# Kernel optimization log

Measured on AMD Instinct MI355X. Metric: run time of the kernel, lower is better.

## Reference

```python
import jax, jax.numpy as jnp
import numpy as np

NUM_LEVELS = 16
LEVEL_DIM = 2
BASE_RES = 16
PER_LEVEL_SCALE = 2.0
LOG2_HASHMAP = 19
INPUT_DIM = 3
N_POINTS = 2_000_000
B = 262144


def _compute_offsets():
    offsets = []
    off = 0
    max_params = 2 ** LOG2_HASHMAP
    for i in range(NUM_LEVELS):
        res = int(np.ceil(BASE_RES * PER_LEVEL_SCALE ** i))
        p = min(max_params, (res + 1) ** INPUT_DIM)  # align_corners=False -> res+1 verts per axis
        p = int(np.ceil(p / 8) * 8)
        offsets.append(off)
        off += p
    offsets.append(off)
    return offsets

OFFSETS = _compute_offsets()
TOTAL_PARAMS = OFFSETS[-1]  # 7131240
PRIMES = (1, 2654435761, 805459861)  # instant-ngp fast_hash primes for D=3
CORNER_BITS = np.array([[(c >> d) & 1 for d in range(3)] for c in range(8)], dtype=np.int32)  # [8,3]


def _build_table(embeddings, fs_embeddings, scatter_index):
    # scatter_add point embeddings (and counts) into grid vertices, then blend
    sums = jnp.zeros((TOTAL_PARAMS, LEVEL_DIM), embeddings.dtype).at[scatter_index].add(embeddings)
    counts = jnp.zeros((TOTAL_PARAMS,), embeddings.dtype).at[scatter_index].add(1.0)
    sel = jnp.minimum(counts, 1.0)[:, None]
    num = jnp.maximum(counts, 1.0)[:, None]
    return (sums / num) * sel + fs_embeddings * (1.0 - sel)


def _grid_encode(x, table):
    # x: [B,3] in [0,1]; table: [TOTAL_PARAMS, C]. Multi-res hash grid, linear interp,
    # align_corners=False (matches torch-ngp grid_encode CUDA kernel).
    S = np.log2(PER_LEVEL_SCALE)
    bits_i = jnp.asarray(CORNER_BITS)                 # [8,3] int
    bits_f = jnp.asarray(CORNER_BITS, dtype=x.dtype)  # [8,3] float
    outs = []
    for level in range(NUM_LEVELS):
        scale = np.exp2(level * S) * BASE_RES - 1.0
        resolution = int(np.ceil(scale)) + 1
        hashmap_size = OFFSETS[level + 1] - OFFSETS[level]
        pos = x * scale + 0.5  # align_corners=False offset
        pos_grid = jnp.floor(pos)
        frac = pos - pos_grid                                  # [B,3]
        corner = pos_grid.astype(jnp.int32)[:, None, :] + bits_i  # [B,8,3]
        stride = (resolution + 1) ** 3
        if stride > hashmap_size:
            # hashed level: xor of per-dim prime products, uint32 wraparound
            cu = corner.astype(jnp.uint32)
            idx = (cu[..., 0] * jnp.uint32(PRIMES[0])) ^ \
                  (cu[..., 1] * jnp.uint32(PRIMES[1])) ^ \
                  (cu[..., 2] * jnp.uint32(PRIMES[2]))
            idx = (idx % jnp.uint32(hashmap_size)).astype(jnp.int32)
        else:
            # dense level: row-major index with stride (res+1)
            r1 = resolution + 1
            idx = (corner[..., 0] + corner[..., 1] * r1 + corner[..., 2] * (r1 * r1)) % hashmap_size
        vals = table[idx + OFFSETS[level]]  # [B,8,C] gather
        w = jnp.prod(jnp.where(bits_f > 0, frac[:, None, :], 1.0 - frac[:, None, :]), axis=-1)  # [B,8]
        outs.append(jnp.einsum('bk,bkc->bc', w, vals))
    return jnp.concatenate(outs, axis=-1)  # [B, L*C]


def setup_inputs() -> dict:
    key = jax.random.key(0)
    k1, k2, k3, k4 = jax.random.split(key, 4)
    std = 1e-4  # reset_parameters() uniform(-1e-4, 1e-4)
    inputs = jax.random.uniform(k1, (B, 3), jnp.float32, minval=-1.0, maxval=1.0)
    embeddings = jax.random.uniform(k2, (N_POINTS, LEVEL_DIM), jnp.float32, minval=-std, maxval=std)
    fs_embeddings = jax.random.uniform(k3, (TOTAL_PARAMS, LEVEL_DIM), jnp.float32, minval=-std, maxval=std)
    scatter_index = jax.random.randint(k4, (N_POINTS,), 0, TOTAL_PARAMS, dtype=jnp.int32)
    return {"inputs": inputs, "embeddings": embeddings, "fs_embeddings": fs_embeddings,
            "scatter_index": scatter_index, "bound": 1}


def reference(inputs, embeddings, fs_embeddings, scatter_index, bound):
    table = _build_table(embeddings, fs_embeddings, scatter_index)
    x = (inputs + bound) / (2.0 * bound)  # map to [0,1]
    return _grid_encode(x, table)  # [B, NUM_LEVELS*LEVEL_DIM]
```

## Files before the change

kernel.cpp:

```cpp
#include <hip/hip_runtime.h>

#define TOTAL_PARAMS 7131240
#define NLEVELS 16
#define NB 262144
#define HASH_MASK 0x7FFFF

#define SF2 5115000.0f
#define CF 1e-4f

__constant__ int c_off[NLEVELS] = {
    0, 4920, 40864, 315496, 839784, 1364072, 1888360, 2412648,
    2936936, 3461224, 3985512, 4509800, 5034088, 5558376, 6082664, 6606952};

typedef float vfloat2 __attribute__((ext_vector_type(2)));
typedef float vfloat4 __attribute__((ext_vector_type(4)));
typedef unsigned vuint2 __attribute__((ext_vector_type(2)));
typedef int vint2 __attribute__((ext_vector_type(2)));

__global__ __launch_bounds__(256) void scatter_kernel(
    const vfloat4* __restrict__ emb2, const vint2* __restrict__ sidx2,
    unsigned* __restrict__ accum, int n) {
    int i = blockIdx.x * 256 + threadIdx.x;
    int base = i * 2;
    if (base >= n) return;
    if (base + 1 < n) {
        vint2 idx = __builtin_nontemporal_load(&sidx2[i]);
        vfloat4 e = __builtin_nontemporal_load(&emb2[i]);
        unsigned qx0 = __float2uint_rn((e.x + CF) * SF2);
        unsigned qy0 = __float2uint_rn((e.y + CF) * SF2);
        unsigned qx1 = __float2uint_rn((e.z + CF) * SF2);
        unsigned qy1 = __float2uint_rn((e.w + CF) * SF2);
        atomicAdd(&accum[idx.x], (1u << 28) | (qx0 << 14) | qy0);
        atomicAdd(&accum[idx.y], (1u << 28) | (qx1 << 14) | qy1);
    } else {
        const int* sidx = (const int*)sidx2;
        const vfloat2* emb = (const vfloat2*)emb2;
        int idx = sidx[base];
        vfloat2 e = emb[base];
        unsigned qx = __float2uint_rn((e.x + CF) * SF2);
        unsigned qy = __float2uint_rn((e.y + CF) * SF2);
        atomicAdd(&accum[idx], (1u << 28) | (qx << 14) | qy);
    }
}

__device__ __forceinline__ unsigned short f2bf(float f) {
    unsigned u = __builtin_bit_cast(unsigned, f);
    return (unsigned short)((u + 0x7FFFu + ((u >> 16) & 1u)) >> 16);
}

__global__ __launch_bounds__(256) void finalize_kernel(
    const unsigned* __restrict__ accum, const vfloat4* __restrict__ fs2,
    unsigned long long* __restrict__ table2, int npairs) {
    int i = blockIdx.x * 256 + threadIdx.x;
    if (i >= npairs) return;
    vuint2 a = __builtin_nontemporal_load((const vuint2*)(accum + 2 * i));
    unsigned c0 = a.x >> 28, c1 = a.y >> 28;
    vfloat4 f = {0.0f, 0.0f, 0.0f, 0.0f};
    if ((c0 == 0u) | (c1 == 0u)) f = __builtin_nontemporal_load(&fs2[i]);
    float rx0, ry0, rx1, ry1;
    if (c0 == 0u) {
        rx0 = f.x; ry0 = f.y;
    } else {
        float inv = 1.0f / ((float)c0 * SF2);
        rx0 = (float)((a.x >> 14) & 0x3FFFu) * inv - CF;
        ry0 = (float)(a.x & 0x3FFFu) * inv - CF;
    }
    if (c1 == 0u) {
        rx1 = f.z; ry1 = f.w;
    } else {
        float inv = 1.0f / ((float)c1 * SF2);
        rx1 = (float)((a.y >> 14) & 0x3FFFu) * inv - CF;
        ry1 = (float)(a.y & 0x3FFFu) * inv - CF;
    }
    unsigned lo = (unsigned)f2bf(rx0) | ((unsigned)f2bf(ry0) << 16);
    unsigned hi = (unsigned)f2bf(rx1) | ((unsigned)f2bf(ry1) << 16);
    table2[i] = (unsigned long long)lo | ((unsigned long long)hi << 32);
}

template <bool DENSE>
__device__ __forceinline__ vfloat2 level_interp(
    float px, float py, float pz, int l, const unsigned* __restrict__ table_bf) {
    int res = 16 << l;
    float scale = (float)(res - 1);
    float posx = px * scale + 0.5f;
    float posy = py * scale + 0.5f;
    float posz = pz * scale + 0.5f;
    float gx = floorf(posx), gy = floorf(posy), gz = floorf(posz);
    float fx = posx - gx, fy = posy - gy, fz = posz - gz;
    int ix = (int)gx, iy = (int)gy, iz = (int)gz;

    const unsigned* __restrict__ tb = table_bf + c_off[l];

    unsigned tyz[4];
    if (DENSE) {
        unsigned r1u = (unsigned)(res + 1);
        unsigned r1sq = r1u * r1u;
        unsigned ty0 = (unsigned)iy * r1u;
        unsigned tz0 = (unsigned)iz * r1sq;
        tyz[0] = ty0 + tz0;
        tyz[1] = ty0 + r1u + tz0;
        tyz[2] = ty0 + tz0 + r1sq;
        tyz[3] = ty0 + r1u + tz0 + r1sq;
    } else {
        unsigned ty0 = (unsigned)iy * 2654435761u;
        unsigned ty1 = ty0 + 2654435761u;
        unsigned tz0 = (unsigned)iz * 805459861u;
        unsigned tz1 = tz0 + 805459861u;
        tyz[0] = ty0 ^ tz0;
        tyz[1] = ty1 ^ tz0;
        tyz[2] = ty0 ^ tz1;
        tyz[3] = ty1 ^ tz1;
    }

    unsigned i0[4], i1[4];
    vuint2 P[4];
#pragma unroll
    for (int c = 0; c < 4; ++c) {
        if (DENSE) {
            i0[c] = tyz[c] + (unsigned)ix;
            i1[c] = i0[c] + 1u;
        } else {
            i0[c] = ((unsigned)ix ^ tyz[c]) & HASH_MASK;
            i1[c] = (((unsigned)ix + 1u) ^ tyz[c]) & HASH_MASK;
        }
        P[c] = *(const vuint2*)(tb + (i0[c] & ~1u));
    }
    unsigned vX[4];
#pragma unroll
    for (int c = 0; c < 4; ++c) {
        vX[c] = 0u;
        if (i1[c] != (i0[c] ^ 1u)) vX[c] = tb[i1[c]];
    }

    float wy0 = 1.0f - fy, wz0 = 1.0f - fz;
    float wyzv[4];
    wyzv[0] = wy0 * wz0;
    wyzv[1] = fy * wz0;
    wyzv[2] = wy0 * fz;
    wyzv[3] = fy * fz;
    float wx0 = 1.0f - fx;
    float ax = 0.0f, ay = 0.0f;
#pragma unroll
    for (int c = 0; c < 4; ++c) {
        unsigned lo = P[c].x, hi = P[c].y;
        bool odd = (i0[c] & 1u) != 0u;
        unsigned v0 = odd ? hi : lo;
        unsigned vo = odd ? lo : hi;
        unsigned v1 = (i1[c] == (i0[c] ^ 1u)) ? vo : vX[c];
        float v0x = __builtin_bit_cast(float, v0 << 16);
        float v0y = __builtin_bit_cast(float, v0 & 0xFFFF0000u);
        float v1x = __builtin_bit_cast(float, v1 << 16);
        float v1y = __builtin_bit_cast(float, v1 & 0xFFFF0000u);
        float w = wyzv[c];
        ax += w * (wx0 * v0x + fx * v1x);
        ay += w * (wx0 * v0y + fx * v1y);
    }
    vfloat2 r;
    r.x = ax;
    r.y = ay;
    return r;
}

__global__ __launch_bounds__(256) void encode_hash_kernel(
    const float* __restrict__ x, const int* __restrict__ bound_p,
    const unsigned* __restrict__ table_bf, vfloat2* __restrict__ lm) {
    int l = 15 - (blockIdx.x >> 10);
    int b = ((blockIdx.x & 1023) << 8) + threadIdx.x;

    float bound = (float)bound_p[0];
    float denom = 2.0f * bound;
    float px = (x[b * 3 + 0] + bound) / denom;
    float py = (x[b * 3 + 1] + bound) / denom;
    float pz = (x[b * 3 + 2] + bound) / denom;

    vfloat2 o = level_interp<false>(px, py, pz, l, table_bf);
    __builtin_nontemporal_store(o, &lm[(l - 3) * NB + b]);
}

__global__ __launch_bounds__(256) void finish_kernel(
    const float* __restrict__ x, const int* __restrict__ bound_p,
    const unsigned* __restrict__ table_bf, const vfloat2* __restrict__ lm,
    float* __restrict__ out) {
    int b = blockIdx.x * 256 + threadIdx.x;

    float bound = (float)bound_p[0];
    float denom = 2.0f * bound;
    float px = (x[b * 3 + 0] + bound) / denom;
    float py = (x[b * 3 + 1] + bound) / denom;
    float pz = (x[b * 3 + 2] + bound) / denom;

    float row[2 * NLEVELS];

#pragma unroll
    for (int lev = 0; lev < 13; ++lev) {
        vfloat2 v = lm[lev * NB + b];
        row[2 * (lev + 3)] = v.x;
        row[2 * (lev + 3) + 1] = v.y;
    }
#pragma unroll
    for (int l = 0; l < 3; ++l) {
        vfloat2 o = level_interp<true>(px, py, pz, l, table_bf);
        row[2 * l] = o.x;
        row[2 * l + 1] = o.y;
    }

    vfloat4* op = (vfloat4*)&out[b * 32];
#pragma unroll
    for (int k = 0; k < 8; ++k) {
        vfloat4 o;
        o.x = row[4 * k + 0];
        o.y = row[4 * k + 1];
        o.z = row[4 * k + 2];
        o.w = row[4 * k + 3];
        op[k] = o;
    }
}

extern "C" void kernel_launch(void* const* d_in, const int* in_sizes, int n_in,
                              void* d_out, int out_size, void* d_ws, size_t ws_size,
                              hipStream_t stream) {
    const float* x     = (const float*)d_in[0];
    const float* emb   = (const float*)d_in[1];
    const float* fs    = (const float*)d_in[2];
    const int*   sidx  = (const int*)d_in[3];
    const int*   bound = (const int*)d_in[4];

    unsigned* accum    = (unsigned*)d_ws;
    unsigned* table_bf = accum + TOTAL_PARAMS;
    vfloat2*  lm       = (vfloat2*)d_ws;

    int npts = in_sizes[3];
    int B = in_sizes[0] / 3;

    (void)hipMemsetAsync(d_ws, 0, (size_t)TOTAL_PARAMS * sizeof(unsigned), stream);

    int npair_pts = (npts + 1) / 2;
    scatter_kernel<<<(npair_pts + 255) / 256, 256, 0, stream>>>(
        (const vfloat4*)emb, (const vint2*)sidx, accum, npts);

    int npairs = TOTAL_PARAMS / 2;
    finalize_kernel<<<(npairs + 255) / 256, 256, 0, stream>>>(
        accum, (const vfloat4*)fs, (unsigned long long*)table_bf, npairs);

    encode_hash_kernel<<<13 * (B / 256), 256, 0, stream>>>(
        x, bound, table_bf, lm);

    finish_kernel<<<B / 256, 256, 0, stream>>>(
        x, bound, table_bf, lm, (float*)d_out);
}
```

Baseline: 330.1 us.

## Precompute normalized inputs, process two points per thread, simplify corner gathers

Folds input normalization into the scatter launch as extra blocks that write padded float4 normalized coordinates, so the encode and finish kernels load one aligned vector instead of three strided floats plus a divide. The hash encode kernel now handles two points per thread with explicit occupancy bounds, to raise memory-level parallelism on the random table gathers. The paired 64-bit gather with a conditional extra load is replaced by eight independent 32-bit loads, which removes branches but issues more load instructions. The trade is an extra workspace buffer and higher register pressure per thread.

```diff
diff --git a/kernel.cpp b/kernel.cpp
--- a/kernel.cpp
+++ b/kernel.cpp
@@ -17,9 +17,24 @@
 typedef unsigned vuint2 __attribute__((ext_vector_type(2)));
 typedef int vint2 __attribute__((ext_vector_type(2)));
 
-__global__ __launch_bounds__(256) void scatter_kernel(
+__global__ __launch_bounds__(256) void scatter_prep_kernel(
     const vfloat4* __restrict__ emb2, const vint2* __restrict__ sidx2,
-    unsigned* __restrict__ accum, int n) {
+    unsigned* __restrict__ accum, int n, int nsb,
+    const float* __restrict__ x, const int* __restrict__ bound_p,
+    vfloat4* __restrict__ xn, int B) {
+    if ((int)blockIdx.x >= nsb) {
+        int p = ((int)blockIdx.x - nsb) * 256 + threadIdx.x;
+        if (p >= B) return;
+        float bound = (float)bound_p[0];
+        float denom = 2.0f * bound;
+        vfloat4 o;
+        o.x = (x[p * 3 + 0] + bound) / denom;
+        o.y = (x[p * 3 + 1] + bound) / denom;
+        o.z = (x[p * 3 + 2] + bound) / denom;
+        o.w = 0.0f;
+        xn[p] = o;
+        return;
+    }
     int i = blockIdx.x * 256 + threadIdx.x;
     int base = i * 2;
     if (base >= n) return;
@@ -87,7 +102,7 @@
     float posz = pz * scale + 0.5f;
     float gx = floorf(posx), gy = floorf(posy), gz = floorf(posz);
     float fx = posx - gx, fy = posy - gy, fz = posz - gz;
-    int ix = (int)gx, iy = (int)gy, iz = (int)gz;
+    unsigned ix = (unsigned)(int)gx, iy = (unsigned)(int)gy, iz = (unsigned)(int)gz;
 
     const unsigned* __restrict__ tb = table_bf + c_off[l];
 
@@ -95,63 +110,41 @@
     if (DENSE) {
         unsigned r1u = (unsigned)(res + 1);
         unsigned r1sq = r1u * r1u;
-        unsigned ty0 = (unsigned)iy * r1u;
-        unsigned tz0 = (unsigned)iz * r1sq;
+        unsigned ty0 = iy * r1u, tz0 = iz * r1sq;
         tyz[0] = ty0 + tz0;
         tyz[1] = ty0 + r1u + tz0;
         tyz[2] = ty0 + tz0 + r1sq;
         tyz[3] = ty0 + r1u + tz0 + r1sq;
     } else {
-        unsigned ty0 = (unsigned)iy * 2654435761u;
-        unsigned ty1 = ty0 + 2654435761u;
-        unsigned tz0 = (unsigned)iz * 805459861u;
-        unsigned tz1 = tz0 + 805459861u;
+        unsigned ty0 = iy * 2654435761u, ty1 = ty0 + 2654435761u;
+        unsigned tz0 = iz * 805459861u, tz1 = tz0 + 805459861u;
         tyz[0] = ty0 ^ tz0;
         tyz[1] = ty1 ^ tz0;
         tyz[2] = ty0 ^ tz1;
         tyz[3] = ty1 ^ tz1;
     }
 
-    unsigned i0[4], i1[4];
-    vuint2 P[4];
-#pragma unroll
-    for (int c = 0; c < 4; ++c) {
-        if (DENSE) {
-            i0[c] = tyz[c] + (unsigned)ix;
-            i1[c] = i0[c] + 1u;
-        } else {
-            i0[c] = ((unsigned)ix ^ tyz[c]) & HASH_MASK;
-            i1[c] = (((unsigned)ix + 1u) ^ tyz[c]) & HASH_MASK;
-        }
-        P[c] = *(const vuint2*)(tb + (i0[c] & ~1u));
-    }
-    unsigned vX[4];
-#pragma unroll
-    for (int c = 0; c < 4; ++c) {
-        vX[c] = 0u;
-        if (i1[c] != (i0[c] ^ 1u)) vX[c] = tb[i1[c]];
+    unsigned v[8];
+#pragma unroll
+    for (int c = 0; c < 8; ++c) {
+        unsigned cx = ix + (unsigned)(c & 1);
+        unsigned idx;
+        if (DENSE) idx = cx + tyz[c >> 1];
+        else       idx = (cx ^ tyz[c >> 1]) & HASH_MASK;
+        v[c] = tb[idx];
     }
 
     float wy0 = 1.0f - fy, wz0 = 1.0f - fz;
-    float wyzv[4];
-    wyzv[0] = wy0 * wz0;
-    wyzv[1] = fy * wz0;
-    wyzv[2] = wy0 * fz;
-    wyzv[3] = fy * fz;
+    float wyz[4] = {wy0 * wz0, fy * wz0, wy0 * fz, fy * fz};
     float wx0 = 1.0f - fx;
     float ax = 0.0f, ay = 0.0f;
 #pragma unroll
-    for (int c = 0; c < 4; ++c) {
-        unsigned lo = P[c].x, hi = P[c].y;
-        bool odd = (i0[c] & 1u) != 0u;
-        unsigned v0 = odd ? hi : lo;
-        unsigned vo = odd ? lo : hi;
-        unsigned v1 = (i1[c] == (i0[c] ^ 1u)) ? vo : vX[c];
-        float v0x = __builtin_bit_cast(float, v0 << 16);
-        float v0y = __builtin_bit_cast(float, v0 & 0xFFFF0000u);
-        float v1x = __builtin_bit_cast(float, v1 << 16);
-        float v1y = __builtin_bit_cast(float, v1 & 0xFFFF0000u);
-        float w = wyzv[c];
+    for (int c2 = 0; c2 < 4; ++c2) {
+        float v0x = __builtin_bit_cast(float, v[2 * c2] << 16);
+        float v0y = __builtin_bit_cast(float, v[2 * c2] & 0xFFFF0000u);
+        float v1x = __builtin_bit_cast(float, v[2 * c2 + 1] << 16);
+        float v1y = __builtin_bit_cast(float, v[2 * c2 + 1] & 0xFFFF0000u);
+        float w = wyz[c2];
         ax += w * (wx0 * v0x + fx * v1x);
         ay += w * (wx0 * v0y + fx * v1y);
     }
@@ -161,33 +154,86 @@
     return r;
 }
 
-__global__ __launch_bounds__(256) void encode_hash_kernel(
-    const float* __restrict__ x, const int* __restrict__ bound_p,
-    const unsigned* __restrict__ table_bf, vfloat2* __restrict__ lm) {
-    int l = 15 - (blockIdx.x >> 10);
-    int b = ((blockIdx.x & 1023) << 8) + threadIdx.x;
-
-    float bound = (float)bound_p[0];
-    float denom = 2.0f * bound;
-    float px = (x[b * 3 + 0] + bound) / denom;
-    float py = (x[b * 3 + 1] + bound) / denom;
-    float pz = (x[b * 3 + 2] + bound) / denom;
-
-    vfloat2 o = level_interp<false>(px, py, pz, l, table_bf);
-    __builtin_nontemporal_store(o, &lm[(l - 3) * NB + b]);
-}
-
-__global__ __launch_bounds__(256) void finish_kernel(
-    const float* __restrict__ x, const int* __restrict__ bound_p,
-    const unsigned* __restrict__ table_bf, const vfloat2* __restrict__ lm,
-    float* __restrict__ out) {
+struct v2x2 { vfloat2 a, b; };
+
+__device__ __forceinline__ void hash_idx8(
+    float px, float py, float pz, float scale,
+    unsigned idx[8], float* fx, float* fy, float* fz) {
+    float posx = px * scale + 0.5f;
+    float posy = py * scale + 0.5f;
+    float posz = pz * scale + 0.5f;
+    float gx = floorf(posx), gy = floorf(posy), gz = floorf(posz);
+    *fx = posx - gx; *fy = posy - gy; *fz = posz - gz;
+    unsigned ix = (unsigned)(int)gx, iy = (unsigned)(int)gy, iz = (unsigned)(int)gz;
+    unsigned ty0 = iy * 2654435761u, ty1 = ty0 + 2654435761u;
+    unsigned tz0 = iz * 805459861u, tz1 = tz0 + 805459861u;
+    unsigned tyz[4] = {ty0 ^ tz0, ty1 ^ tz0, ty0 ^ tz1, ty1 ^ tz1};
+#pragma unroll
+    for (int c = 0; c < 8; ++c)
+        idx[c] = ((ix + (unsigned)(c & 1)) ^ tyz[c >> 1]) & HASH_MASK;
+}
+
+__device__ __forceinline__ vfloat2 wsum8(
+    const unsigned v[8], float fx, float fy, float fz) {
+    float wy0 = 1.0f - fy, wz0 = 1.0f - fz;
+    float wyz[4] = {wy0 * wz0, fy * wz0, wy0 * fz, fy * fz};
+    float wx0 = 1.0f - fx;
+    float ax = 0.0f, ay = 0.0f;
+#pragma unroll
+    for (int c2 = 0; c2 < 4; ++c2) {
+        float v0x = __builtin_bit_cast(float, v[2 * c2] << 16);
+        float v0y = __builtin_bit_cast(float, v[2 * c2] & 0xFFFF0000u);
+        float v1x = __builtin_bit_cast(float, v[2 * c2 + 1] << 16);
+        float v1y = __builtin_bit_cast(float, v[2 * c2 + 1] & 0xFFFF0000u);
+        float w = wyz[c2];
+        ax += w * (wx0 * v0x + fx * v1x);
+        ay += w * (wx0 * v0y + fx * v1y);
+    }
+    vfloat2 r;
+    r.x = ax;
+    r.y = ay;
+    return r;
+}
+
+__global__ __launch_bounds__(256, 6) void encode_hash_kernel(
+    const vfloat4* __restrict__ xn, const unsigned* __restrict__ table_bf,
+    vfloat2* __restrict__ lm) {
+    int l = 15 - ((int)blockIdx.x >> 9);
+    int b0 = (((int)blockIdx.x & 511) << 9) + (int)threadIdx.x;
+    int b1 = b0 + 256;
+
+    vfloat4 pA = xn[b0];
+    vfloat4 pB = xn[b1];
+
+    int res = 16 << l;
+    float scale = (float)(res - 1);
+    const unsigned* __restrict__ tb = table_bf + c_off[l];
+
+    unsigned iA[8], iB[8];
+    float fAx, fAy, fAz, fBx, fBy, fBz;
+    hash_idx8(pA.x, pA.y, pA.z, scale, iA, &fAx, &fAy, &fAz);
+    hash_idx8(pB.x, pB.y, pB.z, scale, iB, &fBx, &fBy, &fBz);
+
+    unsigned vA[8], vB[8];
+#pragma unroll
+    for (int c = 0; c < 8; ++c) vA[c] = tb[iA[c]];
+#pragma unroll
+    for (int c = 0; c < 8; ++c) vB[c] = tb[iB[c]];
+
+    vfloat2 oA = wsum8(vA, fAx, fAy, fAz);
+    vfloat2 oB = wsum8(vB, fBx, fBy, fBz);
+
+    vfloat2* dst = &lm[(l - 3) * NB];
+    __builtin_nontemporal_store(oA, dst + b0);
+    __builtin_nontemporal_store(oB, dst + b1);
+}
+
+__global__ __launch_bounds__(256, 4) void finish_kernel(
+    const vfloat4* __restrict__ xn, const unsigned* __restrict__ table_bf,
+    const vfloat2* __restrict__ lm, float* __restrict__ out) {
     int b = blockIdx.x * 256 + threadIdx.x;
 
-    float bound = (float)bound_p[0];
-    float denom = 2.0f * bound;
-    float px = (x[b * 3 + 0] + bound) / denom;
-    float py = (x[b * 3 + 1] + bound) / denom;
-    float pz = (x[b * 3 + 2] + bound) / denom;
+    vfloat4 p = xn[b];
 
     float row[2 * NLEVELS];
 
@@ -199,7 +245,7 @@
     }
 #pragma unroll
     for (int l = 0; l < 3; ++l) {
-        vfloat2 o = level_interp<true>(px, py, pz, l, table_bf);
+        vfloat2 o = level_interp<true>(p.x, p.y, p.z, l, table_bf);
         row[2 * l] = o.x;
         row[2 * l + 1] = o.y;
     }
@@ -227,6 +273,7 @@
 
     unsigned* accum    = (unsigned*)d_ws;
     unsigned* table_bf = accum + TOTAL_PARAMS;
+    vfloat4*  xn       = (vfloat4*)(table_bf + TOTAL_PARAMS);
     vfloat2*  lm       = (vfloat2*)d_ws;
 
     int npts = in_sizes[3];
@@ -235,16 +282,19 @@
     (void)hipMemsetAsync(d_ws, 0, (size_t)TOTAL_PARAMS * sizeof(unsigned), stream);
 
     int npair_pts = (npts + 1) / 2;
-    scatter_kernel<<<(npair_pts + 255) / 256, 256, 0, stream>>>(
-        (const vfloat4*)emb, (const vint2*)sidx, accum, npts);
+    int nsb = (npair_pts + 255) / 256;
+    int npb = (B + 255) / 256;
+    scatter_prep_kernel<<<nsb + npb, 256, 0, stream>>>(
+        (const vfloat4*)emb, (const vint2*)sidx, accum, npts, nsb,
+        x, bound, xn, B);
 
     int npairs = TOTAL_PARAMS / 2;
     finalize_kernel<<<(npairs + 255) / 256, 256, 0, stream>>>(
         accum, (const vfloat4*)fs, (unsigned long long*)table_bf, npairs);
 
-    encode_hash_kernel<<<13 * (B / 256), 256, 0, stream>>>(
-        x, bound, table_bf, lm);
+    encode_hash_kernel<<<13 * (B / 512), 256, 0, stream>>>(
+        xn, table_bf, lm);
 
     finish_kernel<<<B / 256, 256, 0, stream>>>(
-        x, bound, table_bf, lm, (float*)d_out);
-}
+        xn, table_bf, lm, (float*)d_out);
+}
```

Measured after the change: 319.3 us. -3.3%, faster.
